# Performance work log

Hardware: AMD Instinct MI355X
Metric: run time of the kernel (lower is better)

## Reference

```python
import jax, jax.numpy as jnp
import numpy as np

NUM_FEATURES = 20480
NUM_ACC = 128
BATCH = 4096
SPARSITY_P = 0.0015  # ~30 active features per position, like real NNUE


def setup_inputs() -> dict:
    key = jax.random.key(0)
    kw, kb, k1, k2, k3, k4 = jax.random.split(key, 6)
    # sparse binary one-hot-per-piece feature vectors
    white = (jax.random.uniform(kw, (BATCH, NUM_FEATURES)) < SPARSITY_P).astype(jnp.float32)
    black = (jax.random.uniform(kb, (BATCH, NUM_FEATURES)) < SPARSITY_P).astype(jnp.float32)
    psqt_w = jax.random.normal(k1, (2, NUM_FEATURES), dtype=jnp.float32) * 0.02
    acc_w = jax.random.normal(k2, (NUM_ACC, NUM_FEATURES), dtype=jnp.float32) * 0.02
    acc_b = jax.random.normal(k3, (NUM_ACC,), dtype=jnp.float32) * 0.02
    out_w = jax.random.normal(k4, (2, NUM_ACC), dtype=jnp.float32) * 0.1
    return {"white": white, "black": black, "psqt_w": psqt_w,
            "acc_w": acc_w, "acc_b": acc_b, "out_w": out_w}


def _side(x, psqt_w, acc_w, acc_b, out_w):
    # psqt: [B,2]; accumulator: [B,128]; CReLU then Linear(128->2, no bias)
    psqt = x @ psqt_w.T                              # [B, 2]
    acc = jnp.clip(x @ acc_w.T + acc_b, 0.0, 1.0)    # [B, 128]
    pos = acc @ out_w.T                              # [B, 2]
    return psqt, pos


def reference(white, black, psqt_w, acc_w, acc_b, out_w):
    psqt_w_, pos_w = _side(white, psqt_w, acc_w, acc_b, out_w)
    psqt_b, pos_b = _side(black, psqt_w, acc_w, acc_b, out_w)
    return (psqt_w_ - psqt_b) + (pos_w - pos_b)      # [B, 2]
```

## Files before the change

kernel.cpp:

```cpp
#include <hip/hip_runtime.h>

#define NF   20480
#define NACC 128
#define BATCH 4096
#define MAXI 96

typedef unsigned int uvec4 __attribute__((ext_vector_type(4)));
typedef float        fvec4 __attribute__((ext_vector_type(4)));

__global__ __launch_bounds__(256) void transpose_accw(const float* __restrict__ acc_w,
                                                      float* __restrict__ accT) {
    __shared__ float tile[NACC][33];
    const int t  = threadIdx.x;
    const int f0 = blockIdx.x * 32;
    const int fl = t & 31;
    const int cr = t >> 5;
    #pragma unroll
    for (int i = 0; i < 16; ++i) {
        int cc = i * 8 + cr;
        tile[cc][fl] = acc_w[(size_t)cc * NF + f0 + fl];
    }
    __syncthreads();
    const int c  = t & 127;
    const int fr = t >> 7;
    #pragma unroll
    for (int i = 0; i < 16; ++i) {
        int ff = i * 2 + fr;
        accT[(size_t)(f0 + ff) * NACC + c] = tile[c][ff];
    }
}

#define PROCV(u, base)                                                          \
    if (u.x | u.y | u.z | u.w) {                                                \
        if (u.x) { int p = atomicAdd(cnt, 1); if (p < MAXI) idx[p] = (base) + 0; } \
        if (u.y) { int p = atomicAdd(cnt, 1); if (p < MAXI) idx[p] = (base) + 1; } \
        if (u.z) { int p = atomicAdd(cnt, 1); if (p < MAXI) idx[p] = (base) + 2; } \
        if (u.w) { int p = atomicAdd(cnt, 1); if (p < MAXI) idx[p] = (base) + 3; } \
    }

__global__ __launch_bounds__(256) void nnue_main(
    const float* __restrict__ white,
    const float* __restrict__ black,
    const float* __restrict__ psqt_w,
    const float* __restrict__ accT,
    const float* __restrict__ acc_b,
    const float* __restrict__ out_w,
    float* __restrict__ out)
{
    __shared__ int   s_cnt[2];
    __shared__ int   s_idx[2][MAXI];
    __shared__ fvec4 s_part[2][4][32];
    __shared__ float s_red[8];

    const int t    = threadIdx.x;
    const int b    = blockIdx.x;
    const int side = t >> 7;
    const int lt   = t & 127;

    const float bias = acc_b[lt];
    const float ow0  = out_w[lt];
    const float ow1  = out_w[NACC + lt];
    const float sgn  = side ? -1.f : 1.f;

    const float* X  = (side ? black : white) + (size_t)b * NF;
    const uvec4* Xv = (const uvec4*)X;

    if (t < 2) s_cnt[t] = 0;
    __syncthreads();

    int* cnt = &s_cnt[side];
    int* idx = s_idx[side];

    #pragma unroll 2
    for (int i = 0; i < 10; ++i) {
        const int v = i * 512 + lt;
        uvec4 a0 = __builtin_nontemporal_load(&Xv[v]);
        uvec4 a1 = __builtin_nontemporal_load(&Xv[v + 128]);
        uvec4 a2 = __builtin_nontemporal_load(&Xv[v + 256]);
        uvec4 a3 = __builtin_nontemporal_load(&Xv[v + 384]);
        if (a0.x|a0.y|a0.z|a0.w | a1.x|a1.y|a1.z|a1.w |
            a2.x|a2.y|a2.z|a2.w | a3.x|a3.y|a3.z|a3.w) {
            PROCV(a0, (v      ) * 4)
            PROCV(a1, (v + 128) * 4)
            PROCV(a2, (v + 256) * 4)
            PROCV(a3, (v + 384) * 4)
        }
    }
    __syncthreads();

    const int n      = min(s_cnt[side], MAXI);
    const int sub    = (t >> 5) & 3;
    const int lane32 = t & 31;
    const int* sIdx  = s_idx[side];

    float ps0 = 0.f, ps1 = 0.f;
    if (lt < n) {
        int f = sIdx[lt];
        ps0 = psqt_w[f];
        ps1 = psqt_w[NF + f];
    }

    fvec4 acc4 = {0.f, 0.f, 0.f, 0.f};
    for (int j = sub; j < n; j += 4) {
        int f = sIdx[j];
        acc4 += *(const fvec4*)&accT[(size_t)f * NACC + lane32 * 4];
    }
    s_part[side][sub][lane32] = acc4;
    __syncthreads();

    const float* sp = (const float*)&s_part[side][0][0];
    float a = sp[0 * NACC + lt] + sp[1 * NACC + lt]
            + sp[2 * NACC + lt] + sp[3 * NACC + lt];
    float h  = fminf(fmaxf(a + bias, 0.f), 1.f);
    float p0 = sgn * (h * ow0 + ps0);
    float p1 = sgn * (h * ow1 + ps1);

    #pragma unroll
    for (int off = 32; off > 0; off >>= 1) {
        p0 += __shfl_down(p0, off, 64);
        p1 += __shfl_down(p1, off, 64);
    }
    if ((t & 63) == 0) { int wv = t >> 6; s_red[wv * 2] = p0; s_red[wv * 2 + 1] = p1; }
    __syncthreads();

    if (t == 0) {
        out[(size_t)b * 2 + 0] = s_red[0] + s_red[2] + s_red[4] + s_red[6];
        out[(size_t)b * 2 + 1] = s_red[1] + s_red[3] + s_red[5] + s_red[7];
    }
}

extern "C" void kernel_launch(void* const* d_in, const int* in_sizes, int n_in,
                              void* d_out, int out_size, void* d_ws, size_t ws_size,
                              hipStream_t stream) {
    const float* white  = (const float*)d_in[0];
    const float* black  = (const float*)d_in[1];
    const float* psqt_w = (const float*)d_in[2];
    const float* acc_w  = (const float*)d_in[3];
    const float* acc_b  = (const float*)d_in[4];
    const float* out_w  = (const float*)d_in[5];
    float* out = (float*)d_out;

    float* accT = (float*)d_ws;

    transpose_accw<<<NF / 32, 256, 0, stream>>>(acc_w, accT);
    nnue_main<<<BATCH, 256, 0, stream>>>(white, black, psqt_w, accT,
                                         acc_b, out_w, out);
}
```

Measured before the change: 609.2 us.

## Store transposed accumulator weights as bf16, ballot-compact indices, prefetch input

Converts the transposed acc_w workspace to bf16, halving the bytes gathered per active feature. Replaces the per-element shared atomics with wavefront ballot compaction, so each wave does one atomic per nonzero column slot. Software-prefetches the next chunk of the dense input row while the current chunk is scanned. The bf16 rounding of weights adds numerical error, and the ballot path runs sixteen ballots per iteration even when a chunk is all zero.

```diff
diff --git a/kernel.cpp b/kernel.cpp
--- a/kernel.cpp
+++ b/kernel.cpp
@@ -1,15 +1,28 @@
 #include <hip/hip_runtime.h>
 
-#define NF   20480
-#define NACC 128
+#define NF    20480
+#define NACC  128
 #define BATCH 4096
-#define MAXI 96
+#define MAXI  96
 
 typedef unsigned int uvec4 __attribute__((ext_vector_type(4)));
+typedef unsigned int uvec2 __attribute__((ext_vector_type(2)));
 typedef float        fvec4 __attribute__((ext_vector_type(4)));
 
+__device__ __forceinline__ float bflo(unsigned int w) {
+    union { unsigned int u; float f; } v; v.u = w << 16; return v.f;
+}
+__device__ __forceinline__ float bfhi(unsigned int w) {
+    union { unsigned int u; float f; } v; v.u = w & 0xFFFF0000u; return v.f;
+}
+__device__ __forceinline__ unsigned short f2bf(float f) {
+    union { float f; unsigned int i; } v; v.f = f;
+    unsigned int x = v.i;
+    return (unsigned short)((x + 0x7FFFu + ((x >> 16) & 1u)) >> 16);
+}
+
 __global__ __launch_bounds__(256) void transpose_accw(const float* __restrict__ acc_w,
-                                                      float* __restrict__ accT) {
+                                                      unsigned short* __restrict__ accT) {
     __shared__ float tile[NACC][33];
     const int t  = threadIdx.x;
     const int f0 = blockIdx.x * 32;
@@ -26,23 +39,39 @@
     #pragma unroll
     for (int i = 0; i < 16; ++i) {
         int ff = i * 2 + fr;
-        accT[(size_t)(f0 + ff) * NACC + c] = tile[c][ff];
+        accT[(size_t)(f0 + ff) * NACC + c] = f2bf(tile[c][ff]);
     }
 }
 
-#define PROCV(u, base)                                                          \
-    if (u.x | u.y | u.z | u.w) {                                                \
-        if (u.x) { int p = atomicAdd(cnt, 1); if (p < MAXI) idx[p] = (base) + 0; } \
-        if (u.y) { int p = atomicAdd(cnt, 1); if (p < MAXI) idx[p] = (base) + 1; } \
-        if (u.z) { int p = atomicAdd(cnt, 1); if (p < MAXI) idx[p] = (base) + 2; } \
-        if (u.w) { int p = atomicAdd(cnt, 1); if (p < MAXI) idx[p] = (base) + 3; } \
+#define BALLOT_COMPACT(d, fidx)                                           \
+    {                                                                     \
+        unsigned long long m = __ballot((d) != 0u);                       \
+        if (m) {                                                          \
+            int pre  = __popcll(m & ((1ull << lane) - 1ull));             \
+            int src  = (int)(__ffsll((unsigned long long)(m)) - 1);       \
+            int base = 0;                                                 \
+            if (lane == src) base = atomicAdd(cnt, __popcll(m));          \
+            base = __shfl(base, src, 64);                                 \
+            int slot = base + pre;                                        \
+            if ((d) && slot < MAXI) idx[slot] = (fidx);                   \
+        }                                                                 \
     }
+
+#define PROC16(c0, c1, c2, c3, fb)                                        \
+    BALLOT_COMPACT(c0.x, (fb) + 0)   BALLOT_COMPACT(c0.y, (fb) + 1)       \
+    BALLOT_COMPACT(c0.z, (fb) + 2)   BALLOT_COMPACT(c0.w, (fb) + 3)       \
+    BALLOT_COMPACT(c1.x, (fb) + 512) BALLOT_COMPACT(c1.y, (fb) + 513)     \
+    BALLOT_COMPACT(c1.z, (fb) + 514) BALLOT_COMPACT(c1.w, (fb) + 515)     \
+    BALLOT_COMPACT(c2.x, (fb) + 1024) BALLOT_COMPACT(c2.y, (fb) + 1025)   \
+    BALLOT_COMPACT(c2.z, (fb) + 1026) BALLOT_COMPACT(c2.w, (fb) + 1027)   \
+    BALLOT_COMPACT(c3.x, (fb) + 1536) BALLOT_COMPACT(c3.y, (fb) + 1537)   \
+    BALLOT_COMPACT(c3.z, (fb) + 1538) BALLOT_COMPACT(c3.w, (fb) + 1539)
 
 __global__ __launch_bounds__(256) void nnue_main(
     const float* __restrict__ white,
     const float* __restrict__ black,
     const float* __restrict__ psqt_w,
-    const float* __restrict__ accT,
+    const unsigned short* __restrict__ accT,
     const float* __restrict__ acc_b,
     const float* __restrict__ out_w,
     float* __restrict__ out)
@@ -56,6 +85,7 @@
     const int b    = blockIdx.x;
     const int side = t >> 7;
     const int lt   = t & 127;
+    const int lane = t & 63;
 
     const float bias = acc_b[lt];
     const float ow0  = out_w[lt];
@@ -71,20 +101,24 @@
     int* cnt = &s_cnt[side];
     int* idx = s_idx[side];
 
-    #pragma unroll 2
+    uvec4 c0 = __builtin_nontemporal_load(&Xv[lt]);
+    uvec4 c1 = __builtin_nontemporal_load(&Xv[lt + 128]);
+    uvec4 c2 = __builtin_nontemporal_load(&Xv[lt + 256]);
+    uvec4 c3 = __builtin_nontemporal_load(&Xv[lt + 384]);
+
+    #pragma unroll 1
     for (int i = 0; i < 10; ++i) {
-        const int v = i * 512 + lt;
-        uvec4 a0 = __builtin_nontemporal_load(&Xv[v]);
-        uvec4 a1 = __builtin_nontemporal_load(&Xv[v + 128]);
-        uvec4 a2 = __builtin_nontemporal_load(&Xv[v + 256]);
-        uvec4 a3 = __builtin_nontemporal_load(&Xv[v + 384]);
-        if (a0.x|a0.y|a0.z|a0.w | a1.x|a1.y|a1.z|a1.w |
-            a2.x|a2.y|a2.z|a2.w | a3.x|a3.y|a3.z|a3.w) {
-            PROCV(a0, (v      ) * 4)
-            PROCV(a1, (v + 128) * 4)
-            PROCV(a2, (v + 256) * 4)
-            PROCV(a3, (v + 384) * 4)
+        uvec4 n0 = {0,0,0,0}, n1 = {0,0,0,0}, n2 = {0,0,0,0}, n3 = {0,0,0,0};
+        if (i < 9) {
+            const int v = (i + 1) * 512 + lt;
+            n0 = __builtin_nontemporal_load(&Xv[v]);
+            n1 = __builtin_nontemporal_load(&Xv[v + 128]);
+            n2 = __builtin_nontemporal_load(&Xv[v + 256]);
+            n3 = __builtin_nontemporal_load(&Xv[v + 384]);
         }
+        const int fb = (i * 512 + lt) * 4;
+        PROC16(c0, c1, c2, c3, fb)
+        c0 = n0; c1 = n1; c2 = n2; c3 = n3;
     }
     __syncthreads();
 
@@ -103,7 +137,9 @@
     fvec4 acc4 = {0.f, 0.f, 0.f, 0.f};
     for (int j = sub; j < n; j += 4) {
         int f = sIdx[j];
-        acc4 += *(const fvec4*)&accT[(size_t)f * NACC + lane32 * 4];
+        uvec2 w = *(const uvec2*)(accT + (size_t)f * NACC + lane32 * 4);
+        acc4.x += bflo(w.x); acc4.y += bfhi(w.x);
+        acc4.z += bflo(w.y); acc4.w += bfhi(w.y);
     }
     s_part[side][sub][lane32] = acc4;
     __syncthreads();
@@ -140,7 +176,7 @@
     const float* out_w  = (const float*)d_in[5];
     float* out = (float*)d_out;
 
-    float* accT = (float*)d_ws;
+    unsigned short* accT = (unsigned short*)d_ws;
 
     transpose_accw<<<NF / 32, 256, 0, stream>>>(acc_w, accT);
     nnue_main<<<BATCH, 256, 0, stream>>>(white, black, psqt_w, accT,
```

After: 607.3 us, median of 2. Within noise of the previous version (-0.3%).
